# Performance work log

Measured on AMD Instinct MI355X. Metric: run time of the kernel, lower is better.

The kernel has to match this reference:

```python
import jax, jax.numpy as jnp
import numpy as np

DIM = 1024


def _combine(e1, e2):
    # associative op for h_t = a_t * h_{t-1} + b_t (inclusive scan, h_0-contrib handled outside)
    a1, b1 = e1
    a2, b2 = e2
    return a1 * a2, b2 + a2 * b1


def setup_inputs() -> dict:
    key = jax.random.key(0)
    ks = jax.random.split(key, 11)
    s = 1.0 / np.sqrt(DIM)
    d = {
        "x": jax.random.normal(ks[0], (4, 4096, DIM), jnp.float32),
        "hidden": jax.random.normal(ks[1], (4, DIM), jnp.float32),
        "Wf": jax.random.uniform(ks[2], (DIM, DIM), jnp.float32, -s, s),
        "bf": jax.random.uniform(ks[3], (DIM,), jnp.float32, -s, s),
        "Wi": jax.random.uniform(ks[4], (DIM, DIM), jnp.float32, -s, s),
        "bi": jax.random.uniform(ks[5], (DIM,), jnp.float32, -s, s),
        "Wig": jax.random.uniform(ks[6], (DIM, DIM), jnp.float32, -s, s),
        "big": jax.random.uniform(ks[7], (DIM,), jnp.float32, -s, s),
        "Wog": jax.random.uniform(ks[8], (DIM, DIM), jnp.float32, -s, s),
        "bog": jax.random.uniform(ks[9], (DIM,), jnp.float32, -s, s),
    }
    return d


def reference(x, hidden, Wf, bf, Wi, bi, Wig, big, Wog, bog):
    # x: [B, L, D], hidden: [B, D]
    forget = jax.nn.sigmoid(jnp.einsum("bld,ed->ble", x, Wf) + bf)
    inp = jnp.tanh(jnp.einsum("bld,ed->ble", x, Wi) + bi) * \
          jax.nn.sigmoid(jnp.einsum("bld,ed->ble", x, Wig) + big)
    # parallel scan of h_t = forget_t * h_{t-1} + inp_t with h_0 = 0
    _, h_inner = jax.lax.associative_scan(_combine, (forget, inp), axis=1)
    # add initial-hidden contribution: hidden * prod_{s<=t} forget_s
    h = h_inner + hidden[:, None, :] * jnp.cumprod(forget, axis=1)
    y = jnp.tanh(h) * jax.nn.sigmoid(jnp.einsum("bld,ed->ble", x, Wog) + bog)
    return y, h[:, -1, :]
```

## Files before the change

kernel.cpp:

```cpp
#include <hip/hip_runtime.h>
#include <hip/hip_bf16.h>
#include <cstdint>
#include <cstddef>

#define DIMD 1024
#define LSEQ 4096
#define BATCH 4
#define MTOT (BATCH*LSEQ)
#define NCHUNK 64
#define CHUNKLEN 64
#define GATE_ELEMS ((size_t)MTOT*DIMD)
#define NTILE_K 32

typedef __bf16 bf16x8 __attribute__((ext_vector_type(8)));
typedef float f32x4 __attribute__((ext_vector_type(4)));

__device__ __forceinline__ unsigned short f2bf(float f) {
    union { float f; uint32_t u; } v; v.f = f;
    uint32_t r = v.u + 0x7fffu + ((v.u >> 16) & 1u);
    return (unsigned short)(r >> 16);
}
__device__ __forceinline__ float bits2f(unsigned short b) {
    union { uint32_t u; float f; } v; v.u = ((uint32_t)b) << 16; return v.f;
}
__device__ __forceinline__ float fsig(float x) {
    return __builtin_amdgcn_rcpf(1.f + __expf(-x));
}
__device__ __forceinline__ float ftanh(float x) {
    return 2.f * fsig(2.f * x) - 1.f;
}

__global__ void cast_all(const float* __restrict__ x,
                         const float* __restrict__ Wf, const float* __restrict__ Wi,
                         const float* __restrict__ Wig, const float* __restrict__ Wog,
                         unsigned short* __restrict__ Xb, unsigned short* __restrict__ Wcat) {
    int b = blockIdx.x;
    const float* src; unsigned short* dst; int lb;
    if (b < 8192) { src = x; dst = Xb; lb = b; }
    else {
        int w = (b - 8192) >> 9;
        lb = (b - 8192) & 511;
        src = (w == 0) ? Wf : (w == 1) ? Wi : (w == 2) ? Wig : Wog;
        dst = Wcat + (size_t)w * DIMD * DIMD;
    }
    int i = (lb * 256 + threadIdx.x) * 8;
    float4 a = *(const float4*)(src + i);
    float4 c = *(const float4*)(src + i + 4);
    uint4 o;
    o.x = (uint32_t)f2bf(a.x) | ((uint32_t)f2bf(a.y) << 16);
    o.y = (uint32_t)f2bf(a.z) | ((uint32_t)f2bf(a.w) << 16);
    o.z = (uint32_t)f2bf(c.x) | ((uint32_t)f2bf(c.y) << 16);
    o.w = (uint32_t)f2bf(c.z) | ((uint32_t)f2bf(c.w) << 16);
    *(uint4*)(dst + i) = o;
}

__global__ __launch_bounds__(512, 4) void gemm_gates_f(
    const unsigned short* __restrict__ Xb,
    const unsigned short* __restrict__ Wcat,
    const float* __restrict__ bf_, const float* __restrict__ bi_,
    const float* __restrict__ big_, const float* __restrict__ bog_,
    unsigned short* __restrict__ F, unsigned short* __restrict__ I,
    unsigned short* __restrict__ OG,
    float* __restrict__ Aagg, float* __restrict__ Bagg)
{
    __shared__ __align__(16) char lds[73728];
    char* ldsA = lds;
    char* ldsB = lds + 24576;

    const int tid = threadIdx.x;
    const int wave = tid >> 6, lane = tid & 63;
    const int wm = wave >> 2, wn = wave & 3;
    const int l15 = lane & 15, l4 = lane >> 4;

    const int wg = blockIdx.x;
    const int xcd = wg & 7, rr = wg >> 3;
    const int mt = xcd * 16 + (rr & 15);
    const int et = rr >> 4;
    const int m0 = mt * 128, e0 = et * 64;

    const int rsw = (l4 ^ ((l15 >> 1) & 3)) << 4;
    const char* ArdBase = ldsA + (wm * 64 + l15) * 64 + rsw;
    const char* BrdBase = ldsB + (wn * 64 + l15) * 64 + rsw;

    const int srow = tid >> 2;
    const int scg  = ((tid & 3) ^ ((srow >> 1) & 3)) * 8;
    const unsigned short* pAsrc = Xb + (size_t)(m0 + srow) * DIMD + scg;
    const unsigned short* pBsrc0 = Wcat + (size_t)((srow >> 6) * 1024 + e0 + (srow & 63)) * DIMD + scg;
    const unsigned short* pBsrc1 = Wcat + (size_t)((2 + (srow >> 6)) * 1024 + e0 + (srow & 63)) * DIMD + scg;

    auto stage3 = [&](int k0, int offA, int offB) {
        __builtin_amdgcn_global_load_lds(
            (const __attribute__((address_space(1))) uint32_t*)(pAsrc + k0),
            (__attribute__((address_space(3))) uint32_t*)(ldsA + offA + (wave << 10)), 16, 0, 0);
        __builtin_amdgcn_global_load_lds(
            (const __attribute__((address_space(1))) uint32_t*)(pBsrc0 + k0),
            (__attribute__((address_space(3))) uint32_t*)(ldsB + offB + (wave << 10)), 16, 0, 0);
        __builtin_amdgcn_global_load_lds(
            (const __attribute__((address_space(1))) uint32_t*)(pBsrc1 + k0),
            (__attribute__((address_space(3))) uint32_t*)(ldsB + offB + 8192 + (wave << 10)), 16, 0, 0);
    };

    f32x4 acc[4][4];
#pragma unroll
    for (int m = 0; m < 4; ++m)
#pragma unroll
        for (int n = 0; n < 4; ++n) acc[m][n] = (f32x4)0.f;

    stage3(0, 0, 0);
    stage3(32, 8192, 16384);

    int offA0 = 0, offA1 = 8192, offA2 = 16384;
    int offB0 = 0, offB1 = 16384, offB2 = 32768;
#pragma unroll 1
    for (int t = 0; t < NTILE_K; ++t) {
        if (t <= NTILE_K - 2) asm volatile("s_waitcnt vmcnt(3)" ::: "memory");
        else                  asm volatile("s_waitcnt vmcnt(0)" ::: "memory");
        __builtin_amdgcn_s_barrier();
        __builtin_amdgcn_sched_barrier(0);

        if (t + 2 < NTILE_K) stage3((t + 2) * 32, offA2, offB2);

        bf16x8 bv[4], avl[2], avh[2];
#pragma unroll
        for (int n = 0; n < 4; ++n)
            bv[n] = *(const bf16x8*)(BrdBase + offB0 + n * 1024);
        avl[0] = *(const bf16x8*)(ArdBase + offA0);
        avl[1] = *(const bf16x8*)(ArdBase + offA0 + 1024);

        __builtin_amdgcn_s_setprio(1);
#pragma unroll
        for (int m = 0; m < 2; ++m)
#pragma unroll
            for (int n = 0; n < 4; ++n)
                acc[m][n] = __builtin_amdgcn_mfma_f32_16x16x32_bf16(avl[m], bv[n], acc[m][n], 0, 0, 0);
        __builtin_amdgcn_s_setprio(0);

        avh[0] = *(const bf16x8*)(ArdBase + offA0 + 2048);
        avh[1] = *(const bf16x8*)(ArdBase + offA0 + 3072);

        __builtin_amdgcn_s_setprio(1);
#pragma unroll
        for (int m = 0; m < 2; ++m)
#pragma unroll
            for (int n = 0; n < 4; ++n)
                acc[2 + m][n] = __builtin_amdgcn_mfma_f32_16x16x32_bf16(avh[m], bv[n], acc[2 + m][n], 0, 0, 0);
        __builtin_amdgcn_s_setprio(0);

        int ta = offA0; offA0 = offA1; offA1 = offA2; offA2 = ta;
        int tb = offB0; offB0 = offB1; offB1 = offB2; offB2 = tb;
    }

    const float* biasg = (wn == 0) ? bf_ : (wn == 1) ? bi_ : (wn == 2) ? big_ : bog_;
    float bvv[4];
#pragma unroll
    for (int nf = 0; nf < 4; ++nf) bvv[nf] = biasg[e0 + nf * 16 + l15];

#pragma unroll
    for (int mf = 0; mf < 4; ++mf)
#pragma unroll
        for (int nf = 0; nf < 4; ++nf)
#pragma unroll
            for (int r = 0; r < 4; ++r) {
                float pre = acc[mf][nf][r] + bvv[nf];
                acc[mf][nf][r] = (wn == 1) ? ftanh(pre) : fsig(pre);
            }

    float* ldsF  = (float*)lds;
    float* ldsSG = (float*)(lds + 32768);
    unsigned short* ldsTIh = (unsigned short*)(lds + 65536);
    __builtin_amdgcn_s_barrier();
    if (wn == 0 || wn == 2) {
        float* dstL = (wn == 0 ? ldsF : ldsSG) + wm * 4096;
#pragma unroll
        for (int mf = 0; mf < 4; ++mf)
#pragma unroll
            for (int nf = 0; nf < 4; ++nf)
#pragma unroll
                for (int r = 0; r < 4; ++r)
                    dstL[(mf * 16 + l4 * 4 + r) * 64 + nf * 16 + l15] = acc[mf][nf][r];
    } else if (wn == 1) {
        unsigned short* tD = ldsTIh + wm * 2048;
#pragma unroll
        for (int mf = 0; mf < 4; ++mf)
#pragma unroll
            for (int nfi = 0; nfi < 2; ++nfi)
#pragma unroll
                for (int r = 0; r < 4; ++r)
                    tD[(mf * 16 + l4 * 4 + r) * 32 + nfi * 16 + l15] = f2bf(acc[mf][2 + nfi][r]);
    }
    asm volatile("s_waitcnt lgkmcnt(0)" ::: "memory");
    __builtin_amdgcn_s_barrier();

    const size_t rowbase = (size_t)(m0 + wm * 64) * DIMD + e0;
    const int gc = (m0 >> 6) + wm;
    if (wn == 0) {
#pragma unroll
        for (int mf = 0; mf < 4; ++mf)
#pragma unroll
            for (int r = 0; r < 4; ++r) {
                size_t ro = rowbase + (size_t)(mf * 16 + l4 * 4 + r) * DIMD;
#pragma unroll
                for (int nf = 0; nf < 4; ++nf)
                    F[ro + nf * 16 + l15] = f2bf(acc[mf][nf][r]);
            }
    } else if (wn == 3) {
#pragma unroll
        for (int mf = 0; mf < 4; ++mf)
#pragma unroll
            for (int r = 0; r < 4; ++r) {
                size_t ro = rowbase + (size_t)(mf * 16 + l4 * 4 + r) * DIMD;
#pragma unroll
                for (int nf = 0; nf < 4; ++nf)
                    OG[ro + nf * 16 + l15] = f2bf(acc[mf][nf][r]);
            }
    } else if (wn == 1) {
        const float* fL  = ldsF  + wm * 4096;
        const float* sgL = ldsSG + wm * 4096;
#pragma unroll
        for (int nf = 0; nf < 2; ++nf) {
            float A = 1.f, Bv = 0.f;
#pragma unroll
            for (int mf = 0; mf < 4; ++mf) {
                float sA = 1.f, sB = 0.f;
#pragma unroll
                for (int r = 0; r < 4; ++r) {
                    int row = mf * 16 + l4 * 4 + r;
                    int ecl = nf * 16 + l15;
                    float fv = fL[row * 64 + ecl];
                    float iv = acc[mf][nf][r] * sgL[row * 64 + ecl];
                    I[rowbase + (size_t)row * DIMD + ecl] = f2bf(iv);
                    sA = fv * sA;
                    sB = __builtin_fmaf(fv, sB, iv);
                }
#pragma unroll
                for (int s = 16; s <= 32; s <<= 1) {
                    float Ap = __shfl_xor(sA, s, 64);
                    float Bp = __shfl_xor(sB, s, 64);
                    bool later = (lane & s) != 0;
                    float aE = later ? Ap : sA, bE = later ? Bp : sB;
                    float aL = later ? sA : Ap, bL = later ? sB : Bp;
                    sA = aE * aL;
                    sB = __builtin_fmaf(aL, bE, bL);
                }
                Bv = __builtin_fmaf(sA, Bv, sB);
                A  = A * sA;
            }
            if (l4 == 0) {
                int e = e0 + nf * 16 + l15;
                Aagg[(size_t)gc * DIMD + e] = A;
                Bagg[(size_t)gc * DIMD + e] = Bv;
            }
        }
    } else {
        const float* fL  = ldsF + wm * 4096;
        const unsigned short* tiL = ldsTIh + wm * 2048;
#pragma unroll
        for (int nfi = 0; nfi < 2; ++nfi) {
            const int nf = 2 + nfi;
            float A = 1.f, Bv = 0.f;
#pragma unroll
            for (int mf = 0; mf < 4; ++mf) {
                float sA = 1.f, sB = 0.f;
#pragma unroll
                for (int r = 0; r < 4; ++r) {
                    int row = mf * 16 + l4 * 4 + r;
                    int ecl = nf * 16 + l15;
                    float fv = fL[row * 64 + ecl];
                    float iv = bits2f(tiL[row * 32 + nfi * 16 + l15]) * acc[mf][nf][r];
                    I[rowbase + (size_t)row * DIMD + ecl] = f2bf(iv);
                    sA = fv * sA;
                    sB = __builtin_fmaf(fv, sB, iv);
                }
#pragma unroll
                for (int s = 16; s <= 32; s <<= 1) {
                    float Ap = __shfl_xor(sA, s, 64);
                    float Bp = __shfl_xor(sB, s, 64);
                    bool later = (lane & s) != 0;
                    float aE = later ? Ap : sA, bE = later ? Bp : sB;
                    float aL = later ? sA : Ap, bL = later ? sB : Bp;
                    sA = aE * aL;
                    sB = __builtin_fmaf(aL, bE, bL);
                }
                Bv = __builtin_fmaf(sA, Bv, sB);
                A  = A * sA;
            }
            if (l4 == 0) {
                int e = e0 + nf * 16 + l15;
                Aagg[(size_t)gc * DIMD + e] = A;
                Bagg[(size_t)gc * DIMD + e] = Bv;
            }
        }
    }
}

__global__ void scan_phase2(const float* __restrict__ Aagg, const float* __restrict__ Bagg,
                            const float* __restrict__ hidden,
                            float* __restrict__ Hstart, float* __restrict__ out_h) {
    int idx = blockIdx.x * blockDim.x + threadIdx.x;
    int b = idx >> 10, d = idx & 1023;
    float h = hidden[b * 1024 + d];
    size_t base = (size_t)b * NCHUNK * DIMD + d;
    float Av[NCHUNK], Bv[NCHUNK];
#pragma unroll
    for (int c = 0; c < NCHUNK; ++c) {
        Av[c] = Aagg[base + (size_t)c * DIMD];
        Bv[c] = Bagg[base + (size_t)c * DIMD];
    }
#pragma unroll
    for (int c = 0; c < NCHUNK; ++c) {
        Hstart[base + (size_t)c * DIMD] = h;
        h = __builtin_fmaf(Av[c], h, Bv[c]);
    }
    out_h[b * 1024 + d] = h;
}

__global__ void scan_phase3(const unsigned short* __restrict__ F,
                            const unsigned short* __restrict__ I,
                            const unsigned short* __restrict__ OG,
                            const float* __restrict__ Hstart, float* __restrict__ y) {
    const int d0 = threadIdx.x * 4;
    const int c = blockIdx.x, b = blockIdx.y;
    size_t ho = ((size_t)b * NCHUNK + c) * DIMD + d0;
    float4 h4 = *(const float4*)(Hstart + ho);
    float h0 = h4.x, h1 = h4.y, h2 = h4.z, h3 = h4.w;
    size_t base = ((size_t)b * LSEQ + (size_t)c * CHUNKLEN) * DIMD + d0;
#pragma unroll 4
    for (int t = 0; t < CHUNKLEN; ++t) {
        size_t off = base + (size_t)t * DIMD;
        ushort4 fv = *(const ushort4*)(F + off);
        ushort4 iv = *(const ushort4*)(I + off);
        ushort4 gv = *(const ushort4*)(OG + off);
        float4 o;
        h0 = __builtin_fmaf(bits2f(fv.x), h0, bits2f(iv.x)); o.x = ftanh(h0) * bits2f(gv.x);
        h1 = __builtin_fmaf(bits2f(fv.y), h1, bits2f(iv.y)); o.y = ftanh(h1) * bits2f(gv.y);
        h2 = __builtin_fmaf(bits2f(fv.z), h2, bits2f(iv.z)); o.z = ftanh(h2) * bits2f(gv.z);
        h3 = __builtin_fmaf(bits2f(fv.w), h3, bits2f(iv.w)); o.w = ftanh(h3) * bits2f(gv.w);
        *(float4*)(y + off) = o;
    }
}

extern "C" void kernel_launch(void* const* d_in, const int* in_sizes, int n_in,
                              void* d_out, int out_size, void* d_ws, size_t ws_size,
                              hipStream_t stream) {
    const float* x      = (const float*)d_in[0];
    const float* hidden = (const float*)d_in[1];
    const float* Wf  = (const float*)d_in[2];
    const float* bf_ = (const float*)d_in[3];
    const float* Wi  = (const float*)d_in[4];
    const float* bi_ = (const float*)d_in[5];
    const float* Wig = (const float*)d_in[6];
    const float* big_= (const float*)d_in[7];
    const float* Wog = (const float*)d_in[8];
    const float* bog_= (const float*)d_in[9];

    char* ws = (char*)d_ws;
    unsigned short* Xb   = (unsigned short*)(ws);
    unsigned short* Wcat = (unsigned short*)(ws + 33554432);
    unsigned short* F    = (unsigned short*)(ws + 41943040);
    unsigned short* I    = (unsigned short*)(ws + 75497472);
    unsigned short* OG   = (unsigned short*)(ws + 109051904);
    float* Aagg   = (float*)(ws + 142606336);
    float* Bagg   = (float*)(ws + 143654912);
    float* Hstart = (float*)(ws + 144703488);

    float* y     = (float*)d_out;
    float* out_h = y + GATE_ELEMS;

    cast_all<<<10240, 256, 0, stream>>>(x, Wf, Wi, Wig, Wog, Xb, Wcat);

    gemm_gates_f<<<2048, 512, 0, stream>>>(Xb, Wcat, bf_, bi_, big_, bog_,
                                           F, I, OG, Aagg, Bagg);

    scan_phase2<<<BATCH * DIMD / 256, 256, 0, stream>>>(Aagg, Bagg, hidden, Hstart, out_h);
    scan_phase3<<<dim3(NCHUNK, BATCH), 256, 0, stream>>>(F, I, OG, Hstart, y);
}
```

Baseline: 212.9 us.

## Switch gate GEMM from 16x16x32 to 32x32x16 MFMA tiles

Replaces the 4x4 grid of 16x16x32 bf16 MFMAs per wave with a 2x2 grid of 32x32x16 MFMAs. LDS fragment reads and the whole epilogue (bias, activation, LDS staging, global stores and the chunk-level scan with shuffles) are remapped to the 32x32 accumulator layout. The aim is fewer MFMA issues and LDS reads per K-step, with better operand reuse. The new register layout changes the store access patterns and may cost more LDS bank conflicts in the epilogue.

```diff
diff --git a/kernel.cpp b/kernel.cpp
--- a/kernel.cpp
+++ b/kernel.cpp
@@ -13,7 +13,7 @@
 #define NTILE_K 32
 
 typedef __bf16 bf16x8 __attribute__((ext_vector_type(8)));
-typedef float f32x4 __attribute__((ext_vector_type(4)));
+typedef float f32x16 __attribute__((ext_vector_type(16)));
 
 __device__ __forceinline__ unsigned short f2bf(float f) {
     union { float f; uint32_t u; } v; v.f = f;
@@ -70,7 +70,7 @@
     const int tid = threadIdx.x;
     const int wave = tid >> 6, lane = tid & 63;
     const int wm = wave >> 2, wn = wave & 3;
-    const int l15 = lane & 15, l4 = lane >> 4;
+    const int l31 = lane & 31, lh = lane >> 5;
 
     const int wg = blockIdx.x;
     const int xcd = wg & 7, rr = wg >> 3;
@@ -78,9 +78,11 @@
     const int et = rr >> 4;
     const int m0 = mt * 128, e0 = et * 64;
 
-    const int rsw = (l4 ^ ((l15 >> 1) & 3)) << 4;
-    const char* ArdBase = ldsA + (wm * 64 + l15) * 64 + rsw;
-    const char* BrdBase = ldsB + (wn * 64 + l15) * 64 + rsw;
+    const int swzr = (l31 >> 1) & 3;
+    const char* ArdK0 = ldsA + (wm * 64 + l31) * 64 + ((lh ^ swzr) << 4);
+    const char* ArdK1 = ldsA + (wm * 64 + l31) * 64 + (((2 + lh) ^ swzr) << 4);
+    const char* BrdK0 = ldsB + (wn * 64 + l31) * 64 + ((lh ^ swzr) << 4);
+    const char* BrdK1 = ldsB + (wn * 64 + l31) * 64 + (((2 + lh) ^ swzr) << 4);
 
     const int srow = tid >> 2;
     const int scg  = ((tid & 3) ^ ((srow >> 1) & 3)) * 8;
@@ -100,11 +102,11 @@
             (__attribute__((address_space(3))) uint32_t*)(ldsB + offB + 8192 + (wave << 10)), 16, 0, 0);
     };
 
-    f32x4 acc[4][4];
-#pragma unroll
-    for (int m = 0; m < 4; ++m)
-#pragma unroll
-        for (int n = 0; n < 4; ++n) acc[m][n] = (f32x4)0.f;
+    f32x16 acc[2][2];
+#pragma unroll
+    for (int mi = 0; mi < 2; ++mi)
+#pragma unroll
+        for (int ni = 0; ni < 2; ++ni) acc[mi][ni] = (f32x16)0.f;
 
     stage3(0, 0, 0);
     stage3(32, 8192, 16384);
@@ -120,30 +122,27 @@
 
         if (t + 2 < NTILE_K) stage3((t + 2) * 32, offA2, offB2);
 
-        bf16x8 bv[4], avl[2], avh[2];
-#pragma unroll
-        for (int n = 0; n < 4; ++n)
-            bv[n] = *(const bf16x8*)(BrdBase + offB0 + n * 1024);
-        avl[0] = *(const bf16x8*)(ArdBase + offA0);
-        avl[1] = *(const bf16x8*)(ArdBase + offA0 + 1024);
+        bf16x8 av[2][2], bv[2][2];
+#pragma unroll
+        for (int mi = 0; mi < 2; ++mi) {
+            av[mi][0] = *(const bf16x8*)(ArdK0 + offA0 + mi * 2048);
+            av[mi][1] = *(const bf16x8*)(ArdK1 + offA0 + mi * 2048);
+        }
+#pragma unroll
+        for (int ni = 0; ni < 2; ++ni) {
+            bv[ni][0] = *(const bf16x8*)(BrdK0 + offB0 + ni * 2048);
+            bv[ni][1] = *(const bf16x8*)(BrdK1 + offB0 + ni * 2048);
+        }
 
         __builtin_amdgcn_s_setprio(1);
 #pragma unroll
-        for (int m = 0; m < 2; ++m)
-#pragma unroll
-            for (int n = 0; n < 4; ++n)
-                acc[m][n] = __builtin_amdgcn_mfma_f32_16x16x32_bf16(avl[m], bv[n], acc[m][n], 0, 0, 0);
-        __builtin_amdgcn_s_setprio(0);
-
-        avh[0] = *(const bf16x8*)(ArdBase + offA0 + 2048);
-        avh[1] = *(const bf16x8*)(ArdBase + offA0 + 3072);
-
-        __builtin_amdgcn_s_setprio(1);
-#pragma unroll
-        for (int m = 0; m < 2; ++m)
-#pragma unroll
-            for (int n = 0; n < 4; ++n)
-                acc[2 + m][n] = __builtin_amdgcn_mfma_f32_16x16x32_bf16(avh[m], bv[n], acc[2 + m][n], 0, 0, 0);
+        for (int kk = 0; kk < 2; ++kk)
+#pragma unroll
+            for (int mi = 0; mi < 2; ++mi)
+#pragma unroll
+                for (int ni = 0; ni < 2; ++ni)
+                    acc[mi][ni] = __builtin_amdgcn_mfma_f32_32x32x16_bf16(
+                        av[mi][kk], bv[ni][kk], acc[mi][ni], 0, 0, 0);
         __builtin_amdgcn_s_setprio(0);
 
         int ta = offA0; offA0 = offA1; offA1 = offA2; offA2 = ta;
@@ -151,18 +150,18 @@
     }
 
     const float* biasg = (wn == 0) ? bf_ : (wn == 1) ? bi_ : (wn == 2) ? big_ : bog_;
-    float bvv[4];
-#pragma unroll
-    for (int nf = 0; nf < 4; ++nf) bvv[nf] = biasg[e0 + nf * 16 + l15];
-
-#pragma unroll
-    for (int mf = 0; mf < 4; ++mf)
-#pragma unroll
-        for (int nf = 0; nf < 4; ++nf)
-#pragma unroll
-            for (int r = 0; r < 4; ++r) {
-                float pre = acc[mf][nf][r] + bvv[nf];
-                acc[mf][nf][r] = (wn == 1) ? ftanh(pre) : fsig(pre);
+    float bvv[2];
+#pragma unroll
+    for (int ni = 0; ni < 2; ++ni) bvv[ni] = biasg[e0 + ni * 32 + l31];
+
+#pragma unroll
+    for (int mi = 0; mi < 2; ++mi)
+#pragma unroll
+        for (int ni = 0; ni < 2; ++ni)
+#pragma unroll
+            for (int r = 0; r < 16; ++r) {
+                float pre = acc[mi][ni][r] + bvv[ni];
+                acc[mi][ni][r] = (wn == 1) ? ftanh(pre) : fsig(pre);
             }
 
     float* ldsF  = (float*)lds;
@@ -172,71 +171,69 @@
     if (wn == 0 || wn == 2) {
         float* dstL = (wn == 0 ? ldsF : ldsSG) + wm * 4096;
 #pragma unroll
-        for (int mf = 0; mf < 4; ++mf)
-#pragma unroll
-            for (int nf = 0; nf < 4; ++nf)
-#pragma unroll
-                for (int r = 0; r < 4; ++r)
-                    dstL[(mf * 16 + l4 * 4 + r) * 64 + nf * 16 + l15] = acc[mf][nf][r];
+        for (int mi = 0; mi < 2; ++mi)
+#pragma unroll
+            for (int q = 0; q < 4; ++q)
+#pragma unroll
+                for (int rq = 0; rq < 4; ++rq) {
+                    int row = mi * 32 + q * 8 + lh * 4 + rq;
+#pragma unroll
+                    for (int ni = 0; ni < 2; ++ni)
+                        dstL[row * 64 + ni * 32 + l31] = acc[mi][ni][q * 4 + rq];
+                }
     } else if (wn == 1) {
         unsigned short* tD = ldsTIh + wm * 2048;
 #pragma unroll
-        for (int mf = 0; mf < 4; ++mf)
-#pragma unroll
-            for (int nfi = 0; nfi < 2; ++nfi)
-#pragma unroll
-                for (int r = 0; r < 4; ++r)
-                    tD[(mf * 16 + l4 * 4 + r) * 32 + nfi * 16 + l15] = f2bf(acc[mf][2 + nfi][r]);
+        for (int mi = 0; mi < 2; ++mi)
+#pragma unroll
+            for (int q = 0; q < 4; ++q)
+#pragma unroll
+                for (int rq = 0; rq < 4; ++rq) {
+                    int row = mi * 32 + q * 8 + lh * 4 + rq;
+                    tD[row * 32 + l31] = f2bf(acc[mi][1][q * 4 + rq]);
+                }
     }
     asm volatile("s_waitcnt lgkmcnt(0)" ::: "memory");
     __builtin_amdgcn_s_barrier();
 
     const size_t rowbase = (size_t)(m0 + wm * 64) * DIMD + e0;
     const int gc = (m0 >> 6) + wm;
-    if (wn == 0) {
-#pragma unroll
-        for (int mf = 0; mf < 4; ++mf)
-#pragma unroll
-            for (int r = 0; r < 4; ++r) {
-                size_t ro = rowbase + (size_t)(mf * 16 + l4 * 4 + r) * DIMD;
-#pragma unroll
-                for (int nf = 0; nf < 4; ++nf)
-                    F[ro + nf * 16 + l15] = f2bf(acc[mf][nf][r]);
-            }
-    } else if (wn == 3) {
-#pragma unroll
-        for (int mf = 0; mf < 4; ++mf)
-#pragma unroll
-            for (int r = 0; r < 4; ++r) {
-                size_t ro = rowbase + (size_t)(mf * 16 + l4 * 4 + r) * DIMD;
-#pragma unroll
-                for (int nf = 0; nf < 4; ++nf)
-                    OG[ro + nf * 16 + l15] = f2bf(acc[mf][nf][r]);
-            }
+    if (wn == 0 || wn == 3) {
+        unsigned short* dstG = (wn == 0) ? F : OG;
+#pragma unroll
+        for (int mi = 0; mi < 2; ++mi)
+#pragma unroll
+            for (int q = 0; q < 4; ++q)
+#pragma unroll
+                for (int rq = 0; rq < 4; ++rq) {
+                    int row = mi * 32 + q * 8 + lh * 4 + rq;
+                    size_t ro = rowbase + (size_t)row * DIMD;
+#pragma unroll
+                    for (int ni = 0; ni < 2; ++ni)
+                        dstG[ro + ni * 32 + l31] = f2bf(acc[mi][ni][q * 4 + rq]);
+                }
     } else if (wn == 1) {
         const float* fL  = ldsF  + wm * 4096;
         const float* sgL = ldsSG + wm * 4096;
-#pragma unroll
-        for (int nf = 0; nf < 2; ++nf) {
-            float A = 1.f, Bv = 0.f;
-#pragma unroll
-            for (int mf = 0; mf < 4; ++mf) {
+        float A = 1.f, Bv = 0.f;
+#pragma unroll
+        for (int mi = 0; mi < 2; ++mi)
+#pragma unroll
+            for (int q = 0; q < 4; ++q) {
                 float sA = 1.f, sB = 0.f;
 #pragma unroll
-                for (int r = 0; r < 4; ++r) {
-                    int row = mf * 16 + l4 * 4 + r;
-                    int ecl = nf * 16 + l15;
-                    float fv = fL[row * 64 + ecl];
-                    float iv = acc[mf][nf][r] * sgL[row * 64 + ecl];
-                    I[rowbase + (size_t)row * DIMD + ecl] = f2bf(iv);
+                for (int rq = 0; rq < 4; ++rq) {
+                    int row = mi * 32 + q * 8 + lh * 4 + rq;
+                    float fv = fL[row * 64 + l31];
+                    float iv = acc[mi][0][q * 4 + rq] * sgL[row * 64 + l31];
+                    I[rowbase + (size_t)row * DIMD + l31] = f2bf(iv);
                     sA = fv * sA;
                     sB = __builtin_fmaf(fv, sB, iv);
                 }
-#pragma unroll
-                for (int s = 16; s <= 32; s <<= 1) {
-                    float Ap = __shfl_xor(sA, s, 64);
-                    float Bp = __shfl_xor(sB, s, 64);
-                    bool later = (lane & s) != 0;
+                {
+                    float Ap = __shfl_xor(sA, 32, 64);
+                    float Bp = __shfl_xor(sB, 32, 64);
+                    bool later = lh != 0;
                     float aE = later ? Ap : sA, bE = later ? Bp : sB;
                     float aL = later ? sA : Ap, bL = later ? sB : Bp;
                     sA = aE * aL;
@@ -245,37 +242,33 @@
                 Bv = __builtin_fmaf(sA, Bv, sB);
                 A  = A * sA;
             }
-            if (l4 == 0) {
-                int e = e0 + nf * 16 + l15;
-                Aagg[(size_t)gc * DIMD + e] = A;
-                Bagg[(size_t)gc * DIMD + e] = Bv;
-            }
+        if (lh == 0) {
+            int e = e0 + l31;
+            Aagg[(size_t)gc * DIMD + e] = A;
+            Bagg[(size_t)gc * DIMD + e] = Bv;
         }
     } else {
         const float* fL  = ldsF + wm * 4096;
         const unsigned short* tiL = ldsTIh + wm * 2048;
-#pragma unroll
-        for (int nfi = 0; nfi < 2; ++nfi) {
-            const int nf = 2 + nfi;
-            float A = 1.f, Bv = 0.f;
-#pragma unroll
-            for (int mf = 0; mf < 4; ++mf) {
+        float A = 1.f, Bv = 0.f;
+#pragma unroll
+        for (int mi = 0; mi < 2; ++mi)
+#pragma unroll
+            for (int q = 0; q < 4; ++q) {
                 float sA = 1.f, sB = 0.f;
 #pragma unroll
-                for (int r = 0; r < 4; ++r) {
-                    int row = mf * 16 + l4 * 4 + r;
-                    int ecl = nf * 16 + l15;
-                    float fv = fL[row * 64 + ecl];
-                    float iv = bits2f(tiL[row * 32 + nfi * 16 + l15]) * acc[mf][nf][r];
-                    I[rowbase + (size_t)row * DIMD + ecl] = f2bf(iv);
+                for (int rq = 0; rq < 4; ++rq) {
+                    int row = mi * 32 + q * 8 + lh * 4 + rq;
+                    float fv = fL[row * 64 + 32 + l31];
+                    float iv = bits2f(tiL[row * 32 + l31]) * acc[mi][1][q * 4 + rq];
+                    I[rowbase + (size_t)row * DIMD + 32 + l31] = f2bf(iv);
                     sA = fv * sA;
                     sB = __builtin_fmaf(fv, sB, iv);
                 }
-#pragma unroll
-                for (int s = 16; s <= 32; s <<= 1) {
-                    float Ap = __shfl_xor(sA, s, 64);
-                    float Bp = __shfl_xor(sB, s, 64);
-                    bool later = (lane & s) != 0;
+                {
+                    float Ap = __shfl_xor(sA, 32, 64);
+                    float Bp = __shfl_xor(sB, 32, 64);
+                    bool later = lh != 0;
                     float aE = later ? Ap : sA, bE = later ? Bp : sB;
                     float aL = later ? sA : Ap, bL = later ? sB : Bp;
                     sA = aE * aL;
@@ -284,11 +277,10 @@
                 Bv = __builtin_fmaf(sA, Bv, sB);
                 A  = A * sA;
             }
-            if (l4 == 0) {
-                int e = e0 + nf * 16 + l15;
-                Aagg[(size_t)gc * DIMD + e] = A;
-                Bagg[(size_t)gc * DIMD + e] = Bv;
-            }
+        if (lh == 0) {
+            int e = e0 + 32 + l31;
+            Aagg[(size_t)gc * DIMD + e] = A;
+            Bagg[(size_t)gc * DIMD + e] = Bv;
         }
     }
 }
```

Measured after the change: 229.7 us. 7.9% more time.
